# Performance work log

Hardware: AMD Instinct MI355X
Metric: run time of the kernel (lower is better)

Reference implementation:

```python
import jax, jax.numpy as jnp
import numpy as np

B, CIN, COUT, H, W, K = 4, 3, 16, 256, 256, 5
PAD = K // 2  # replicate padding keeps spatial size


def _dilation_sum(x, w):
    """Learnable dilation, channel_merge_mode='sum'.
    x: (B,Cin,H,W), w: (Cout,Cin,K,K).
    out[b,o,i,j] = sum_c max_{di,dj} ( x_pad[b,c,i+di,j+dj] + w[o,c,di,dj] )
    """
    xp = jnp.pad(x, ((0, 0), (0, 0), (PAD, PAD), (PAD, PAD)), mode='edge')
    acc = jnp.full((x.shape[0], w.shape[0], x.shape[1], H, W), -jnp.inf, dtype=x.dtype)
    for di in range(K):  # fixed small kernel loop (unrolled), not a data-dim loop
        for dj in range(K):
            win = xp[:, :, di:di + H, dj:dj + W]                     # (B,Cin,H,W)
            cand = win[:, None] + w[None, :, :, di, dj][:, :, :, None, None]  # (B,Cout,Cin,H,W)
            acc = jnp.maximum(acc, cand)
    return acc.sum(axis=2)  # merge over input channels -> (B,Cout,H,W)


def _erosion_identity(y, w):
    """Learnable erosion, channel_merge_mode='identity' (each channel independent).
    y: (B,Cout,H,W), w: (Cout,K,K).
    out[b,o,i,j] = min_{di,dj} ( y_pad[b,o,i+di,j+dj] - w[o,di,dj] )
    """
    yp = jnp.pad(y, ((0, 0), (0, 0), (PAD, PAD), (PAD, PAD)), mode='edge')
    acc = jnp.full(y.shape, jnp.inf, dtype=y.dtype)
    for di in range(K):
        for dj in range(K):
            acc = jnp.minimum(acc, yp[:, :, di:di + H, dj:dj + W] - w[None, :, di, dj, None, None])
    return acc


def setup_inputs() -> dict:
    key = jax.random.key(0)
    k1, k2, k3 = jax.random.split(key, 3)
    x = jax.random.normal(k1, (B, CIN, H, W), dtype=jnp.float32)
    w_d = jax.random.normal(k2, (COUT, CIN, K, K), dtype=jnp.float32) * 0.05
    w_e = jax.random.normal(k3, (COUT, K, K), dtype=jnp.float32) * 0.05
    return {"x": x, "w_d": w_d, "w_e": w_e}


def reference(x, w_d, w_e):
    # Closing = dilation (max-plus, sum merge) followed by erosion (min-plus, identity merge)
    dilated = _dilation_sum(x, w_d)
    return _erosion_identity(dilated, w_e)
```

## Files before the change

### kernel.cpp

```cpp
#include <hip/hip_runtime.h>
#include <float.h>


namespace {
constexpr int HH = 256, WW = 256, CI = 3;
constexpr int TT = 32;
constexpr int XS = 44;
constexpr int XCH = 40 * XS;
constexpr int DS = 44;
}

__device__ __forceinline__ float4 dapp(float4 m, float4 A, float4 B, const float* w5) {
    const float w0 = w5[0], w1 = w5[1], w2 = w5[2], w3 = w5[3], w4 = w5[4];
    {   float u = fmaxf(fmaxf(A.x + w0, A.y + w1), A.z + w2);
        m.x = fmaxf(m.x, fmaxf(fmaxf(u, A.w + w3), B.x + w4)); }
    {   float u = fmaxf(fmaxf(A.y + w0, A.z + w1), A.w + w2);
        m.y = fmaxf(m.y, fmaxf(fmaxf(u, B.x + w3), B.y + w4)); }
    {   float u = fmaxf(fmaxf(A.z + w0, A.w + w1), B.x + w2);
        m.z = fmaxf(m.z, fmaxf(fmaxf(u, B.y + w3), B.z + w4)); }
    {   float u = fmaxf(fmaxf(A.w + w0, B.x + w1), B.y + w2);
        m.w = fmaxf(m.w, fmaxf(fmaxf(u, B.z + w3), B.w + w4)); }
    return m;
}

__device__ __forceinline__ void add4(float4& a, float4 m) {
    a.x += m.x; a.y += m.y; a.z += m.z; a.w += m.w;
}

__global__ __launch_bounds__(256, 5)
void closing_v5(const float* __restrict__ x, const float* __restrict__ wd,
                const float* __restrict__ we, float* __restrict__ out) {
    __shared__ __align__(16) float sx[CI * XCH];
    __shared__ __align__(16) float sdil[36 * DS];

    const int tid = threadIdx.x;
    const int bx = blockIdx.x, by = blockIdx.y, z = blockIdx.z;
    const int o = z & 15, b = z >> 4;
    const int i0 = by * TT, j0 = bx * TT;
    const float* xb = x + (size_t)b * (CI * HH * WW);

#pragma unroll
    for (int k = 0; k < 19; ++k) {
        const int idx = tid + (k << 8);
        if (idx < CI * 1600) {
            const int c   = idx / 1600;
            const int rem = idx - c * 1600;
            const int rr  = rem / 40;
            const int cc  = rem - rr * 40;
            int gi = i0 - 4 + rr; gi = min(max(gi, 0), HH - 1);
            int gj = j0 - 4 + cc; gj = min(max(gj, 0), WW - 1);
            sx[c * XCH + rr * XS + cc] = xb[c * (HH * WW) + (gi << 8) + gj];
        }
    }
    __syncthreads();

    if (tid < 108) {
        const int q = tid / 9, s = tid - q * 9;
        float4 acc0 = {0,0,0,0}, acc1 = acc0, acc2 = acc0;
#pragma unroll
        for (int c = 0; c < CI; ++c) {
            const float* wr = wd + (o * CI + c) * 25;
            const float* base = &sx[c * XCH + (3 * q) * XS + 4 * s];
            const float NEG = -FLT_MAX;
            float4 m0 = {NEG,NEG,NEG,NEG}, m1 = m0, m2 = m0;
#pragma unroll
            for (int dr = 0; dr < 7; ++dr) {
                const float4 A = *(const float4*)(base + dr * XS);
                const float4 B = *(const float4*)(base + dr * XS + 4);
                if (dr <= 4)            m0 = dapp(m0, A, B, wr + dr * 5);
                if (dr >= 1 && dr <= 5) m1 = dapp(m1, A, B, wr + (dr - 1) * 5);
                if (dr >= 2)            m2 = dapp(m2, A, B, wr + (dr - 2) * 5);
            }
            add4(acc0, m0); add4(acc1, m1); add4(acc2, m2);
        }

        if (bx == 0 && s == 0) {
            acc0.x = acc0.y = acc0.z;  acc1.x = acc1.y = acc1.z;  acc2.x = acc2.y = acc2.z;
        }
        if (bx == 7 && s == 8) {
            acc0.z = acc0.w = acc0.y;  acc1.z = acc1.w = acc1.y;  acc2.z = acc2.w = acc2.y;
        }
        float4 w0 = acc0, w1 = acc1, w2 = acc2;
        if (by == 0 && q == 0)  { w0 = acc2; w1 = acc2; }
        if (by == 7 && q == 11) { w1 = acc0; w2 = acc0; }
        float* dp = &sdil[(3 * q) * DS + 4 * s];
        *(float4*)(dp)          = w0;
        *(float4*)(dp + DS)     = w1;
        *(float4*)(dp + 2 * DS) = w2;
    }
    __syncthreads();

    {
        const int r = tid >> 3, s = tid & 7;
        const float* ew = we + o * 25;
        const float* eb = &sdil[r * DS + 4 * s];
        const float PF = FLT_MAX;
        float4 r0 = {PF, PF, PF, PF};
#pragma unroll
        for (int dd = 0; dd < 5; ++dd) {
            const float4 A = *(const float4*)(eb + dd * DS);
            const float4 B = *(const float4*)(eb + dd * DS + 4);
            const float e0 = ew[dd*5+0], e1 = ew[dd*5+1], e2 = ew[dd*5+2],
                        e3 = ew[dd*5+3], e4 = ew[dd*5+4];
            {   float u = fminf(fminf(A.x - e0, A.y - e1), A.z - e2);
                r0.x = fminf(r0.x, fminf(fminf(u, A.w - e3), B.x - e4)); }
            {   float u = fminf(fminf(A.y - e0, A.z - e1), A.w - e2);
                r0.y = fminf(r0.y, fminf(fminf(u, B.x - e3), B.y - e4)); }
            {   float u = fminf(fminf(A.z - e0, A.w - e1), B.x - e2);
                r0.z = fminf(r0.z, fminf(fminf(u, B.y - e3), B.z - e4)); }
            {   float u = fminf(fminf(A.w - e0, B.x - e1), B.y - e2);
                r0.w = fminf(r0.w, fminf(fminf(u, B.z - e3), B.w - e4)); }
        }
        *(float4*)&out[((size_t)z << 16) + ((size_t)(i0 + r) << 8) + j0 + 4 * s] = r0;
    }
}

extern "C" void kernel_launch(void* const* d_in, const int* in_sizes, int n_in,
                              void* d_out, int out_size, void* d_ws, size_t ws_size,
                              hipStream_t stream) {
    const float* x  = (const float*)d_in[0];
    const float* wd = (const float*)d_in[1];
    const float* we = (const float*)d_in[2];
    float* out = (float*)d_out;

    dim3 grid(WW / TT, HH / TT, 4 * 16);
    closing_v5<<<grid, dim3(256), 0, stream>>>(x, wd, we, out);
}
```

Before: 97.57 us.

## Switch morphology pipeline to packed fp16 and widen tiles to 64 columns

Converts input tiles to packed half2 in shared memory and computes both the dilation and the erosion with packed fp16 max/min/add ops, using bit-shift lane realignment. Tile width doubles to 64 columns, the global loads become float4 with edge-replicate handling, and the replicate padding is reorganised. The aim is to halve LDS traffic and double ALU throughput per instruction. It lowers numerical precision to fp16 for intermediate sums, which may exceed the tolerance.

```diff
diff --git a/kernel.cpp b/kernel.cpp
--- a/kernel.cpp
+++ b/kernel.cpp
@@ -1,117 +1,153 @@
 #include <hip/hip_runtime.h>
-#include <float.h>
 
+
+typedef _Float16 h2 __attribute__((ext_vector_type(2)));
 
 namespace {
 constexpr int HH = 256, WW = 256, CI = 3;
-constexpr int TT = 32;
-constexpr int XS = 44;
-constexpr int XCH = 40 * XS;
-constexpr int DS = 44;
+constexpr int XS2 = 36;
+constexpr int CH2 = 40 * XS2;
+constexpr int DS2 = 36;
 }
 
-__device__ __forceinline__ float4 dapp(float4 m, float4 A, float4 B, const float* w5) {
-    const float w0 = w5[0], w1 = w5[1], w2 = w5[2], w3 = w5[3], w4 = w5[4];
-    {   float u = fmaxf(fmaxf(A.x + w0, A.y + w1), A.z + w2);
-        m.x = fmaxf(m.x, fmaxf(fmaxf(u, A.w + w3), B.x + w4)); }
-    {   float u = fmaxf(fmaxf(A.y + w0, A.z + w1), A.w + w2);
-        m.y = fmaxf(m.y, fmaxf(fmaxf(u, B.x + w3), B.y + w4)); }
-    {   float u = fmaxf(fmaxf(A.z + w0, A.w + w1), B.x + w2);
-        m.z = fmaxf(m.z, fmaxf(fmaxf(u, B.y + w3), B.z + w4)); }
-    {   float u = fmaxf(fmaxf(A.w + w0, B.x + w1), B.y + w2);
-        m.w = fmaxf(m.w, fmaxf(fmaxf(u, B.z + w3), B.w + w4)); }
-    return m;
+struct __align__(16) h2x4 { h2 a, b, c, d; };
+struct __align__(8)  h2x2 { h2 a, b; };
+
+__device__ __forceinline__ h2 pmax(h2 a, h2 b) { return __builtin_elementwise_max(a, b); }
+__device__ __forceinline__ h2 pmin(h2 a, h2 b) { return __builtin_elementwise_min(a, b); }
+
+__device__ __forceinline__ h2 shr1(h2 lo, h2 hi) {
+    unsigned a = __builtin_bit_cast(unsigned, lo);
+    unsigned b = __builtin_bit_cast(unsigned, hi);
+    unsigned r = (a >> 16) | (b << 16);
+    return __builtin_bit_cast(h2, r);
 }
 
-__device__ __forceinline__ void add4(float4& a, float4 m) {
-    a.x += m.x; a.y += m.y; a.z += m.z; a.w += m.w;
+__device__ __forceinline__ void dtaps(h2& m0, h2& m1, h2& m2, h2& m3,
+                                      const h2x4 A, const h2x2 B,
+                                      h2 w0, h2 w1, h2 w2, h2 w3, h2 w4) {
+    const h2 s0 = shr1(A.a, A.b), s1 = shr1(A.b, A.c), s2 = shr1(A.c, A.d),
+             s3 = shr1(A.d, B.a), s4 = shr1(B.a, B.b);
+    m0 = pmax(m0, pmax(pmax(A.a + w0, s0 + w1), pmax(A.b + w2, pmax(s1 + w3, A.c + w4))));
+    m1 = pmax(m1, pmax(pmax(A.b + w0, s1 + w1), pmax(A.c + w2, pmax(s2 + w3, A.d + w4))));
+    m2 = pmax(m2, pmax(pmax(A.c + w0, s2 + w1), pmax(A.d + w2, pmax(s3 + w3, B.a + w4))));
+    m3 = pmax(m3, pmax(pmax(A.d + w0, s3 + w1), pmax(B.a + w2, pmax(s4 + w3, B.b + w4))));
 }
 
-__global__ __launch_bounds__(256, 5)
-void closing_v5(const float* __restrict__ x, const float* __restrict__ wd,
+__device__ __forceinline__ void etaps(h2& m0, h2& m1, h2& m2, h2& m3,
+                                      const h2x4 A, const h2x2 B,
+                                      h2 w0, h2 w1, h2 w2, h2 w3, h2 w4) {
+    const h2 s0 = shr1(A.a, A.b), s1 = shr1(A.b, A.c), s2 = shr1(A.c, A.d),
+             s3 = shr1(A.d, B.a), s4 = shr1(B.a, B.b);
+    m0 = pmin(m0, pmin(pmin(A.a + w0, s0 + w1), pmin(A.b + w2, pmin(s1 + w3, A.c + w4))));
+    m1 = pmin(m1, pmin(pmin(A.b + w0, s1 + w1), pmin(A.c + w2, pmin(s2 + w3, A.d + w4))));
+    m2 = pmin(m2, pmin(pmin(A.c + w0, s2 + w1), pmin(A.d + w2, pmin(s3 + w3, B.a + w4))));
+    m3 = pmin(m3, pmin(pmin(A.d + w0, s3 + w1), pmin(B.a + w2, pmin(s4 + w3, B.b + w4))));
+}
+
+__global__ __launch_bounds__(256, 6)
+void closing_v7(const float* __restrict__ x, const float* __restrict__ wd,
                 const float* __restrict__ we, float* __restrict__ out) {
-    __shared__ __align__(16) float sx[CI * XCH];
-    __shared__ __align__(16) float sdil[36 * DS];
+    __shared__ __align__(16) h2 sx2[CI * CH2 + 8];
+    __shared__ __align__(16) h2 sd2[36 * DS2];
 
     const int tid = threadIdx.x;
     const int bx = blockIdx.x, by = blockIdx.y, z = blockIdx.z;
     const int o = z & 15, b = z >> 4;
-    const int i0 = by * TT, j0 = bx * TT;
+    const int i0 = by * 32, j0 = bx * 64;
     const float* xb = x + (size_t)b * (CI * HH * WW);
 
 #pragma unroll
-    for (int k = 0; k < 19; ++k) {
+    for (int k = 0; k < 9; ++k) {
         const int idx = tid + (k << 8);
-        if (idx < CI * 1600) {
-            const int c   = idx / 1600;
-            const int rem = idx - c * 1600;
-            const int rr  = rem / 40;
-            const int cc  = rem - rr * 40;
-            int gi = i0 - 4 + rr; gi = min(max(gi, 0), HH - 1);
-            int gj = j0 - 4 + cc; gj = min(max(gj, 0), WW - 1);
-            sx[c * XCH + rr * XS + cc] = xb[c * (HH * WW) + (gi << 8) + gj];
+        if (idx < 2160) {
+            const int c   = idx / 720;
+            const int rem = idx - c * 720;
+            const int r   = rem / 18;
+            const int q   = rem - r * 18;
+            const int gi  = min(max(i0 - 4 + r, 0), HH - 1);
+            const int gj0 = j0 - 4 + (q << 2);
+            const float* rowp = xb + c * (HH * WW) + (gi << 8);
+            float4 v;
+            if (gj0 < 0)        { const float t = rowp[0];      v = make_float4(t, t, t, t); }
+            else if (gj0 > 252) { const float t = rowp[WW - 1]; v = make_float4(t, t, t, t); }
+            else                  v = *(const float4*)(rowp + gj0);
+            h2x2 hw;
+            hw.a = h2{(_Float16)v.x, (_Float16)v.y};
+            hw.b = h2{(_Float16)v.z, (_Float16)v.w};
+            *(h2x2*)&sx2[c * CH2 + r * XS2 + (q << 1)] = hw;
         }
     }
     __syncthreads();
 
-    if (tid < 108) {
-        const int q = tid / 9, s = tid - q * 9;
-        float4 acc0 = {0,0,0,0}, acc1 = acc0, acc2 = acc0;
+    for (int t = tid; t < 324; t += 256) {
+        const int rr = t / 9, s = t - rr * 9;
+        const int colh = s << 2;
+        h2 acc0 = (h2)(_Float16)0.f, acc1 = acc0, acc2 = acc0, acc3 = acc0;
 #pragma unroll
         for (int c = 0; c < CI; ++c) {
             const float* wr = wd + (o * CI + c) * 25;
-            const float* base = &sx[c * XCH + (3 * q) * XS + 4 * s];
-            const float NEG = -FLT_MAX;
-            float4 m0 = {NEG,NEG,NEG,NEG}, m1 = m0, m2 = m0;
+            h2 wk[25];
 #pragma unroll
-            for (int dr = 0; dr < 7; ++dr) {
-                const float4 A = *(const float4*)(base + dr * XS);
-                const float4 B = *(const float4*)(base + dr * XS + 4);
-                if (dr <= 4)            m0 = dapp(m0, A, B, wr + dr * 5);
-                if (dr >= 1 && dr <= 5) m1 = dapp(m1, A, B, wr + (dr - 1) * 5);
-                if (dr >= 2)            m2 = dapp(m2, A, B, wr + (dr - 2) * 5);
+            for (int i = 0; i < 25; ++i) wk[i] = (h2)(_Float16)wr[i];
+            h2 m0 = (h2)(_Float16)-60000.f, m1 = m0, m2 = m0, m3 = m0;
+            const int base = c * CH2 + rr * XS2 + colh;
+#pragma unroll
+            for (int r5 = 0; r5 < 5; ++r5) {
+                const h2x4 A = *(const h2x4*)&sx2[base + r5 * XS2];
+                const h2x2 B = *(const h2x2*)&sx2[base + r5 * XS2 + 4];
+                dtaps(m0, m1, m2, m3, A, B,
+                      wk[r5*5+0], wk[r5*5+1], wk[r5*5+2], wk[r5*5+3], wk[r5*5+4]);
             }
-            add4(acc0, m0); add4(acc1, m1); add4(acc2, m2);
+            acc0 = acc0 + m0; acc1 = acc1 + m1; acc2 = acc2 + m2; acc3 = acc3 + m3;
         }
-
-        if (bx == 0 && s == 0) {
-            acc0.x = acc0.y = acc0.z;  acc1.x = acc1.y = acc1.z;  acc2.x = acc2.y = acc2.z;
+        if (bx == 0 && s == 0) acc0 = (h2)acc1.x;
+        if (bx == 3 && s == 8) acc1 = (h2)acc0.y;
+        bool store = true;
+        if (by == 0 && rr < 2)  store = false;
+        if (by == 7 && rr > 33) store = false;
+        if (store) {
+            const int db = rr * DS2 + colh;
+            if (s < 8) { h2x4 w4v = {acc0, acc1, acc2, acc3}; *(h2x4*)&sd2[db] = w4v; }
+            else       { h2x2 w2v = {acc0, acc1};             *(h2x2*)&sd2[db] = w2v; }
+            if (by == 0 && rr == 2) {
+#pragma unroll
+                for (int pr = 0; pr < 2; ++pr) {
+                    const int pb = pr * DS2 + colh;
+                    if (s < 8) { h2x4 w4v = {acc0, acc1, acc2, acc3}; *(h2x4*)&sd2[pb] = w4v; }
+                    else       { h2x2 w2v = {acc0, acc1};             *(h2x2*)&sd2[pb] = w2v; }
+                }
+            }
+            if (by == 7 && rr == 33) {
+#pragma unroll
+                for (int pr = 34; pr < 36; ++pr) {
+                    const int pb = pr * DS2 + colh;
+                    if (s < 8) { h2x4 w4v = {acc0, acc1, acc2, acc3}; *(h2x4*)&sd2[pb] = w4v; }
+                    else       { h2x2 w2v = {acc0, acc1};             *(h2x2*)&sd2[pb] = w2v; }
+                }
+            }
         }
-        if (bx == 7 && s == 8) {
-            acc0.z = acc0.w = acc0.y;  acc1.z = acc1.w = acc1.y;  acc2.z = acc2.w = acc2.y;
-        }
-        float4 w0 = acc0, w1 = acc1, w2 = acc2;
-        if (by == 0 && q == 0)  { w0 = acc2; w1 = acc2; }
-        if (by == 7 && q == 11) { w1 = acc0; w2 = acc0; }
-        float* dp = &sdil[(3 * q) * DS + 4 * s];
-        *(float4*)(dp)          = w0;
-        *(float4*)(dp + DS)     = w1;
-        *(float4*)(dp + 2 * DS) = w2;
     }
     __syncthreads();
 
     {
         const int r = tid >> 3, s = tid & 7;
         const float* ew = we + o * 25;
-        const float* eb = &sdil[r * DS + 4 * s];
-        const float PF = FLT_MAX;
-        float4 r0 = {PF, PF, PF, PF};
+        h2 wk[25];
 #pragma unroll
-        for (int dd = 0; dd < 5; ++dd) {
-            const float4 A = *(const float4*)(eb + dd * DS);
-            const float4 B = *(const float4*)(eb + dd * DS + 4);
-            const float e0 = ew[dd*5+0], e1 = ew[dd*5+1], e2 = ew[dd*5+2],
-                        e3 = ew[dd*5+3], e4 = ew[dd*5+4];
-            {   float u = fminf(fminf(A.x - e0, A.y - e1), A.z - e2);
-                r0.x = fminf(r0.x, fminf(fminf(u, A.w - e3), B.x - e4)); }
-            {   float u = fminf(fminf(A.y - e0, A.z - e1), A.w - e2);
-                r0.y = fminf(r0.y, fminf(fminf(u, B.x - e3), B.y - e4)); }
-            {   float u = fminf(fminf(A.z - e0, A.w - e1), B.x - e2);
-                r0.z = fminf(r0.z, fminf(fminf(u, B.y - e3), B.z - e4)); }
-            {   float u = fminf(fminf(A.w - e0, B.x - e1), B.y - e2);
-                r0.w = fminf(r0.w, fminf(fminf(u, B.z - e3), B.w - e4)); }
+        for (int i = 0; i < 25; ++i) wk[i] = (h2)(_Float16)(-ew[i]);
+        h2 m0 = (h2)(_Float16)60000.f, m1 = m0, m2 = m0, m3 = m0;
+        const int base = r * DS2 + (s << 2);
+#pragma unroll
+        for (int r5 = 0; r5 < 5; ++r5) {
+            const h2x4 A = *(const h2x4*)&sd2[base + r5 * DS2];
+            const h2x2 B = *(const h2x2*)&sd2[base + r5 * DS2 + 4];
+            etaps(m0, m1, m2, m3, A, B,
+                  wk[r5*5+0], wk[r5*5+1], wk[r5*5+2], wk[r5*5+3], wk[r5*5+4]);
         }
-        *(float4*)&out[((size_t)z << 16) + ((size_t)(i0 + r) << 8) + j0 + 4 * s] = r0;
+        float* op = &out[((size_t)z << 16) + ((size_t)(i0 + r) << 8) + j0 + (s << 3)];
+        *(float4*)op       = make_float4((float)m0.x, (float)m0.y, (float)m1.x, (float)m1.y);
+        *(float4*)(op + 4) = make_float4((float)m2.x, (float)m2.y, (float)m3.x, (float)m3.y);
     }
 }
 
@@ -123,6 +159,6 @@
     const float* we = (const float*)d_in[2];
     float* out = (float*)d_out;
 
-    dim3 grid(WW / TT, HH / TT, 4 * 16);
-    closing_v5<<<grid, dim3(256), 0, stream>>>(x, wd, we, out);
+    dim3 grid(4, 8, 64);
+    closing_v7<<<grid, dim3(256), 0, stream>>>(x, wd, we, out);
 }
```

After: 104.2 us. +6.8%, slower.
